# Optimization experiments

Hardware: AMD Instinct MI355X
Metric: run time of the kernel (lower is better)

## Reference

```python
import jax, jax.numpy as jnp
import numpy as np

# Model config (matches init_kwargs)
B, T, D = 2, 2048, 2048
H, KH, F = 16, 4, 8192
HD = D // H            # 128
G = H // KH            # q heads per kv head = 4
EPS = 1e-5


def _ln(x, g, b):
    m = jnp.mean(x, axis=-1, keepdims=True)
    v = jnp.mean((x - m) ** 2, axis=-1, keepdims=True)
    return (x - m) * jax.lax.rsqrt(v + EPS) * g + b


def setup_inputs() -> dict:
    key = jax.random.key(0)
    ks = jax.random.split(key, 8)

    def xav(k, shape):
        lim = (6.0 / (shape[0] + shape[1])) ** 0.5
        return jax.random.uniform(k, shape, jnp.float32, -lim, lim)

    x = jax.random.normal(ks[0], (B, T, D), jnp.float32)
    mask = jnp.tril(jnp.ones((1, 1, T, T), jnp.int32))  # causal
    # Linear weights stored as [in, out] (transpose of torch nn.Linear)
    return {
        "x": x,
        "mask": mask,
        "Wq": xav(ks[1], (D, H * HD)), "bq": jnp.zeros((H * HD,), jnp.float32),
        "Wk": xav(ks[2], (D, KH * HD)), "bk": jnp.zeros((KH * HD,), jnp.float32),
        "Wv": xav(ks[3], (D, KH * HD)), "bv": jnp.zeros((KH * HD,), jnp.float32),
        "Wo": xav(ks[4], (H * HD, D)), "bo": jnp.zeros((D,), jnp.float32),
        "ln1_g": jnp.ones((D,), jnp.float32), "ln1_b": jnp.zeros((D,), jnp.float32),
        "ln2_g": jnp.ones((D,), jnp.float32), "ln2_b": jnp.zeros((D,), jnp.float32),
        "fln_g": jnp.ones((D,), jnp.float32), "fln_b": jnp.zeros((D,), jnp.float32),
        "W1": xav(ks[5], (D, F)), "b1": jnp.zeros((F,), jnp.float32),
        "W2": xav(ks[6], (D, F)), "b2": jnp.zeros((F,), jnp.float32),
        "W3": xav(ks[7], (F, D)), "b3": jnp.zeros((D,), jnp.float32),
    }


def reference(x, mask, Wq, bq, Wk, bk, Wv, bv, Wo, bo,
              ln1_g, ln1_b, ln2_g, ln2_b, fln_g, fln_b,
              W1, b1, W2, b2, W3, b3):
    scale = 1.0 / np.sqrt(HD)
    # --- attention block (pre-LN + residual) ---
    h = _ln(x, ln1_g, ln1_b)
    q = (h @ Wq + bq).reshape(B, T, KH, G, HD)   # q head k*G+g uses kv head k
    k = (h @ Wk + bk).reshape(B, T, KH, HD)
    v = (h @ Wv + bv).reshape(B, T, KH, HD)
    # GQA scores without repeat_interleave: broadcast kv head across group g
    scores = jnp.einsum('btkgd,bskd->bkgts', q, k) * scale  # [B,KH,G,T,T]
    scores = jnp.clip(scores, -100.0, 100.0)
    scores = jnp.where(mask[:, :, None] == 0, -jnp.inf, scores)
    attn = jax.nn.softmax(scores, axis=-1)
    ctx = jnp.einsum('bkgts,bskd->btkgd', attn, v).reshape(B, T, H * HD)
    x = x + (ctx @ Wo + bo)  # dropout is identity in eval
    # --- ln2 then SwiGLU FFN (which has its own internal LN and residual
    # around the *post-ln2* activation, faithful to original) ---
    x = _ln(x, ln2_g, ln2_b)
    r = x
    h2 = _ln(x, fln_g, fln_b)
    g_pre = h2 @ W1 + b1
    gate = g_pre * jax.nn.sigmoid(jnp.clip(g_pre, -10.0, 10.0))
    hidden = h2 @ W2 + b2
    return r + ((gate * hidden) @ W3 + b3)
```

## Files before the change

kernel.cpp:

```cpp
#include <hip/hip_runtime.h>
#include <math.h>
#include <stdint.h>

typedef __bf16 bf16_t;
typedef __bf16 bf16x4 __attribute__((ext_vector_type(4)));
typedef __bf16 bf16x8 __attribute__((ext_vector_type(8)));
typedef float  f32x4  __attribute__((ext_vector_type(4)));

#define D_MODEL 2048
#define T_SEQ   2048
#define BATCH   2
#define NROWS   (BATCH*T_SEQ)
#define NHEAD   16
#define HDIM    128
#define KVH     4
#define KVD     (KVH*HDIM)
#define FDIM    8192
#define QKVN    3072

__device__ __forceinline__ bf16x8 mk8(bf16x4 lo, bf16x4 hi) {
  union { bf16x4 h[2]; bf16x8 v; } u;
  u.h[0] = lo; u.h[1] = hi; return u.v;
}

__device__ __forceinline__ void gl16(const bf16_t* g, bf16_t* l) {
  __builtin_amdgcn_global_load_lds(
      (const uint32_t __attribute__((address_space(1)))*)g,
      (uint32_t __attribute__((address_space(3)))*)l, 16, 0, 0);
}

__global__ __launch_bounds__(256)
void transpose_w(const float* __restrict__ in, bf16_t* __restrict__ outT, int K, int N)
{
  __shared__ __align__(16) bf16_t t[64][72];
  const int tid = threadIdx.x;
  const int k0 = blockIdx.y * 64, n0 = blockIdx.x * 64;
  const int tr = tid >> 4, tc = (tid & 15) * 4;
#pragma unroll
  for (int i = 0; i < 4; ++i) {
    f32x4 v = *(const f32x4*)(in + (size_t)(k0 + tr + 16 * i) * N + n0 + tc);
#pragma unroll
    for (int e = 0; e < 4; ++e) t[tr + 16 * i][tc + e] = (bf16_t)v[e];
  }
  __syncthreads();
#pragma unroll
  for (int s = 0; s < 2; ++s) {
    const int c = s * 256 + tid;
    const int n = c >> 3, c8 = (c & 7) * 8;
    bf16x8 o;
#pragma unroll
    for (int e = 0; e < 8; ++e) o[e] = t[c8 + e][n];
    *(bf16x8*)(outT + (size_t)(n0 + n) * K + k0 + c8) = o;
  }
}

__global__ __launch_bounds__(256)
void concat_bias(const float* __restrict__ a, const float* __restrict__ b,
                 const float* __restrict__ c, float* __restrict__ dst)
{
  const int i = blockIdx.x * 256 + threadIdx.x;
  if (i >= QKVN) return;
  dst[i] = (i < 2048) ? a[i] : (i < 2560) ? b[i - 2048] : c[i - 2560];
}

template<typename TI>
__global__ __launch_bounds__(256)
void ln_kernel(const TI* __restrict__ x, const float* __restrict__ g,
               const float* __restrict__ b, bf16_t* __restrict__ out)
{
  const int row = blockIdx.x;
  const int tid = threadIdx.x;
  const TI* xr = x + (size_t)row * D_MODEL;
  float vals[8];
  if constexpr (sizeof(TI) == 4) {
    f32x4 v0 = *(const f32x4*)(xr + tid * 8);
    f32x4 v1 = *(const f32x4*)(xr + tid * 8 + 4);
#pragma unroll
    for (int e = 0; e < 4; ++e) { vals[e] = v0[e]; vals[4 + e] = v1[e]; }
  } else {
    bf16x8 v = *(const bf16x8*)(xr + tid * 8);
#pragma unroll
    for (int e = 0; e < 8; ++e) vals[e] = (float)v[e];
  }
  float s = 0.f, s2 = 0.f;
#pragma unroll
  for (int e = 0; e < 8; ++e) { s += vals[e]; s2 += vals[e] * vals[e]; }
#pragma unroll
  for (int off = 1; off < 64; off <<= 1) { s += __shfl_xor(s, off); s2 += __shfl_xor(s2, off); }
  __shared__ float red[8];
  const int wid = tid >> 6, lane = tid & 63;
  if (lane == 0) { red[wid] = s; red[4 + wid] = s2; }
  __syncthreads();
  s  = red[0] + red[1] + red[2] + red[3];
  s2 = red[4] + red[5] + red[6] + red[7];
  const float mean = s * (1.f / D_MODEL);
  const float var  = s2 * (1.f / D_MODEL) - mean * mean;
  const float rstd = rsqrtf(var + 1e-5f);
  f32x4 g0 = *(const f32x4*)(g + tid * 8), g1 = *(const f32x4*)(g + tid * 8 + 4);
  f32x4 b0 = *(const f32x4*)(b + tid * 8), b1 = *(const f32x4*)(b + tid * 8 + 4);
  bf16x8 o;
#pragma unroll
  for (int e = 0; e < 4; ++e) {
    o[e]     = (bf16_t)((vals[e]     - mean) * rstd * g0[e] + b0[e]);
    o[4 + e] = (bf16_t)((vals[4 + e] - mean) * rstd * g1[e] + b1[e]);
  }
  *(bf16x8*)(out + (size_t)row * D_MODEL + tid * 8) = o;
}

__global__ __launch_bounds__(256)
void ln2_fused(const bf16_t* __restrict__ x, const float* __restrict__ g2,
               const float* __restrict__ b2, const float* __restrict__ gf,
               const float* __restrict__ bf_, bf16_t* __restrict__ rout,
               bf16_t* __restrict__ hout)
{
  const int row = blockIdx.x;
  const int tid = threadIdx.x;
  const int wid = tid >> 6, lane = tid & 63;
  __shared__ float red[8];
  const bf16_t* xr = x + (size_t)row * D_MODEL;
  bf16x8 v = *(const bf16x8*)(xr + tid * 8);
  float vals[8]; float s = 0.f, s2 = 0.f;
#pragma unroll
  for (int e = 0; e < 8; ++e) { vals[e] = (float)v[e]; s += vals[e]; s2 += vals[e] * vals[e]; }
#pragma unroll
  for (int off = 1; off < 64; off <<= 1) { s += __shfl_xor(s, off); s2 += __shfl_xor(s2, off); }
  if (lane == 0) { red[wid] = s; red[4 + wid] = s2; }
  __syncthreads();
  s  = red[0] + red[1] + red[2] + red[3];
  s2 = red[4] + red[5] + red[6] + red[7];
  float mean = s * (1.f / D_MODEL);
  float var  = s2 * (1.f / D_MODEL) - mean * mean;
  float rstd = rsqrtf(var + 1e-5f);
  f32x4 ga0 = *(const f32x4*)(g2 + tid * 8), ga1 = *(const f32x4*)(g2 + tid * 8 + 4);
  f32x4 ba0 = *(const f32x4*)(b2 + tid * 8), ba1 = *(const f32x4*)(b2 + tid * 8 + 4);
  float y[8];
#pragma unroll
  for (int e = 0; e < 4; ++e) {
    y[e]     = (vals[e]     - mean) * rstd * ga0[e] + ba0[e];
    y[4 + e] = (vals[4 + e] - mean) * rstd * ga1[e] + ba1[e];
  }
  bf16x8 o1;
#pragma unroll
  for (int e = 0; e < 8; ++e) o1[e] = (bf16_t)y[e];
  *(bf16x8*)(rout + (size_t)row * D_MODEL + tid * 8) = o1;
  s = 0.f; s2 = 0.f;
#pragma unroll
  for (int e = 0; e < 8; ++e) { s += y[e]; s2 += y[e] * y[e]; }
#pragma unroll
  for (int off = 1; off < 64; off <<= 1) { s += __shfl_xor(s, off); s2 += __shfl_xor(s2, off); }
  __syncthreads();
  if (lane == 0) { red[wid] = s; red[4 + wid] = s2; }
  __syncthreads();
  s  = red[0] + red[1] + red[2] + red[3];
  s2 = red[4] + red[5] + red[6] + red[7];
  mean = s * (1.f / D_MODEL);
  var  = s2 * (1.f / D_MODEL) - mean * mean;
  rstd = rsqrtf(var + 1e-5f);
  f32x4 gb0 = *(const f32x4*)(gf + tid * 8), gb1 = *(const f32x4*)(gf + tid * 8 + 4);
  f32x4 bb0 = *(const f32x4*)(bf_ + tid * 8), bb1 = *(const f32x4*)(bf_ + tid * 8 + 4);
  bf16x8 o2;
#pragma unroll
  for (int e = 0; e < 4; ++e) {
    o2[e]     = (bf16_t)((y[e]     - mean) * rstd * gb0[e] + bb0[e]);
    o2[4 + e] = (bf16_t)((y[4 + e] - mean) * rstd * gb1[e] + bb1[e]);
  }
  *(bf16x8*)(hout + (size_t)row * D_MODEL + tid * 8) = o2;
}

enum { EPI_NONE = 0, EPI_RES = 1, EPI_SILU = 2, EPI_MUL = 3 };

template<int EPI, int BM_T, typename TE, typename TO>
__global__ __launch_bounds__(512, 2)
void gemm8p(const bf16_t* __restrict__ A, const bf16_t* __restrict__ Bt,
            const float* __restrict__ bias, const TE* __restrict__ extra,
            TO* __restrict__ out, int M, int N, int K)
{
  constexpr int ALs = BM_T / 128;
  constexpr int RF  = BM_T / 32;
  __shared__ __align__(16) bf16_t As[2][2][BM_T * 32];
  __shared__ __align__(16) bf16_t Bs[2][2][256 * 32];
  const int tid = threadIdx.x, lane = tid & 63, wid = tid >> 6;
  const int wr = wid >> 2, wc = wid & 3;
  const int l16 = lane & 15, lq = lane >> 4;
  const int m0 = blockIdx.y * BM_T, n0 = blockIdx.x * 256;

  const bf16_t* aP[ALs]; int aL[ALs];
#pragma unroll
  for (int s = 0; s < ALs; ++s) {
    const int c = s * 512 + tid;
    const int row = c >> 2, pos = c & 3;
    aP[s] = A + (size_t)(m0 + row) * K + (pos ^ ((row >> 1) & 3)) * 8;
    aL[s] = (s * 512 + wid * 64) * 8;
  }
  const bf16_t* bP[2]; int bL[2];
#pragma unroll
  for (int s = 0; s < 2; ++s) {
    const int c = s * 512 + tid;
    const int row = c >> 2, pos = c & 3;
    bP[s] = Bt + (size_t)(n0 + row) * K + (pos ^ ((row >> 1) & 3)) * 8;
    bL[s] = (s * 512 + wid * 64) * 8;
  }

  int offA[RF];
#pragma unroll
  for (int i = 0; i < RF; ++i) {
    const int r = wr * (BM_T / 2) + i * 16 + l16;
    offA[i] = r * 32 + ((lq ^ ((r >> 1) & 3)) * 8);
  }
  int offB[4];
#pragma unroll
  for (int jj = 0; jj < 4; ++jj) {
    const int r = wc * 64 + jj * 16 + l16;
    offB[jj] = r * 32 + ((lq ^ ((r >> 1) & 3)) * 8);
  }

  f32x4 acc[RF][4];
#pragma unroll
  for (int i = 0; i < RF; ++i)
#pragma unroll
    for (int j = 0; j < 4; ++j) acc[i][j] = (f32x4){0.f, 0.f, 0.f, 0.f};

  auto SA = [&](int t, int bb, int kh) {
#pragma unroll
    for (int s = 0; s < ALs; ++s) gl16(aP[s] + t * 64 + kh * 32, &As[bb][kh][aL[s]]);
  };
  auto SB = [&](int t, int bb, int kh) {
#pragma unroll
    for (int s = 0; s < 2; ++s) gl16(bP[s] + t * 64 + kh * 32, &Bs[bb][kh][bL[s]]);
  };
#define BAR_()  __builtin_amdgcn_s_barrier()
#define LGKM_() do { asm volatile("s_waitcnt lgkmcnt(0)" ::: "memory"); \
                     __builtin_amdgcn_sched_barrier(0); } while (0)

  const int nt = K >> 6;
  SA(0, 0, 0); SB(0, 0, 0); SA(0, 0, 1); SB(0, 0, 1);
  if (nt > 1) { SA(1, 1, 0); SB(1, 1, 0); SA(1, 1, 1); }
  if (nt > 2) {
    if constexpr (ALs == 2) asm volatile("s_waitcnt vmcnt(6)" ::: "memory");
    else                    asm volatile("s_waitcnt vmcnt(4)" ::: "memory");
  } else {
    asm volatile("s_waitcnt vmcnt(0)" ::: "memory");
  }
  BAR_();

  for (int t = 0; t < nt; ++t) {
    const int b = t & 1, ob = b ^ 1;
    const bool s1 = (t + 1 < nt), s2 = (t + 2 < nt);
    bf16x8 af[RF], bf0, bf1;
#pragma unroll
    for (int i = 0; i < RF; ++i) af[i] = *(const bf16x8*)(&As[b][0][offA[i]]);
    bf0 = *(const bf16x8*)(&Bs[b][0][offB[0]]);
    bf1 = *(const bf16x8*)(&Bs[b][0][offB[1]]);
    if (s1) SB(t + 1, ob, 1);
    BAR_(); LGKM_();
    __builtin_amdgcn_s_setprio(1);
#pragma unroll
    for (int i = 0; i < RF; ++i) {
      acc[i][0] = __builtin_amdgcn_mfma_f32_16x16x32_bf16(af[i], bf0, acc[i][0], 0, 0, 0);
      acc[i][1] = __builtin_amdgcn_mfma_f32_16x16x32_bf16(af[i], bf1, acc[i][1], 0, 0, 0);
    }
    __builtin_amdgcn_s_setprio(0);
    BAR_();
    bf0 = *(const bf16x8*)(&Bs[b][0][offB[2]]);
    bf1 = *(const bf16x8*)(&Bs[b][0][offB[3]]);
    if (s2) SA(t + 2, b, 0);
    BAR_(); LGKM_();
    __builtin_amdgcn_s_setprio(1);
#pragma unroll
    for (int i = 0; i < RF; ++i) {
      acc[i][2] = __builtin_amdgcn_mfma_f32_16x16x32_bf16(af[i], bf0, acc[i][2], 0, 0, 0);
      acc[i][3] = __builtin_amdgcn_mfma_f32_16x16x32_bf16(af[i], bf1, acc[i][3], 0, 0, 0);
    }
    __builtin_amdgcn_s_setprio(0);
    BAR_();
#pragma unroll
    for (int i = 0; i < RF; ++i) af[i] = *(const bf16x8*)(&As[b][1][offA[i]]);
    bf0 = *(const bf16x8*)(&Bs[b][1][offB[0]]);
    bf1 = *(const bf16x8*)(&Bs[b][1][offB[1]]);
    if (s2) SB(t + 2, b, 0);
    BAR_(); LGKM_();
    __builtin_amdgcn_s_setprio(1);
#pragma unroll
    for (int i = 0; i < RF; ++i) {
      acc[i][0] = __builtin_amdgcn_mfma_f32_16x16x32_bf16(af[i], bf0, acc[i][0], 0, 0, 0);
      acc[i][1] = __builtin_amdgcn_mfma_f32_16x16x32_bf16(af[i], bf1, acc[i][1], 0, 0, 0);
    }
    __builtin_amdgcn_s_setprio(0);
    BAR_();
    bf0 = *(const bf16x8*)(&Bs[b][1][offB[2]]);
    bf1 = *(const bf16x8*)(&Bs[b][1][offB[3]]);
    if (s2) SA(t + 2, b, 1);
    BAR_(); LGKM_();
    __builtin_amdgcn_s_setprio(1);
#pragma unroll
    for (int i = 0; i < RF; ++i) {
      acc[i][2] = __builtin_amdgcn_mfma_f32_16x16x32_bf16(af[i], bf0, acc[i][2], 0, 0, 0);
      acc[i][3] = __builtin_amdgcn_mfma_f32_16x16x32_bf16(af[i], bf1, acc[i][3], 0, 0, 0);
    }
    __builtin_amdgcn_s_setprio(0);
    if (t < nt - 2) {
      if constexpr (ALs == 2) asm volatile("s_waitcnt vmcnt(6)" ::: "memory");
      else                    asm volatile("s_waitcnt vmcnt(4)" ::: "memory");
    } else {
      asm volatile("s_waitcnt vmcnt(0)" ::: "memory");
    }
    BAR_();
  }
#undef BAR_
#undef LGKM_

#pragma unroll
  for (int j = 0; j < 4; ++j) {
    const int col = n0 + wc * 64 + j * 16 + l16;
    const float bb = bias[col];
#pragma unroll
    for (int i = 0; i < RF; ++i) {
      const int row0 = m0 + wr * (BM_T / 2) + i * 16 + lq * 4;
#pragma unroll
      for (int e = 0; e < 4; ++e) {
        const size_t idx = (size_t)(row0 + e) * N + col;
        float vv = acc[i][j][e] + bb;
        if (EPI == EPI_RES)       vv += (float)extra[idx];
        else if (EPI == EPI_SILU) { float c2 = fminf(fmaxf(vv, -10.f), 10.f); vv = vv / (1.f + __expf(-c2)); }
        else if (EPI == EPI_MUL)  vv *= (float)extra[idx];
        out[idx] = (TO)vv;
      }
    }
  }
}

template<int EPI, typename TE, typename TO>
__global__ __launch_bounds__(256)
void gemm_kernel(const bf16_t* __restrict__ A, const float* __restrict__ W,
                 const float* __restrict__ bias, const TE* __restrict__ extra,
                 TO* __restrict__ out, int M, int N, int K)
{
  __shared__ bf16_t As[128][40];
  __shared__ bf16_t Bs[128][40];
  const int tid  = threadIdx.x;
  const int lane = tid & 63, wid = tid >> 6;
  const int wr = wid >> 1, wc = wid & 1;
  const int l16 = lane & 15, lq = lane >> 4;
  const int m0 = blockIdx.y * 128, n0 = blockIdx.x * 128;

  f32x4 acc[4][4];
#pragma unroll
  for (int i = 0; i < 4; ++i)
#pragma unroll
    for (int j = 0; j < 4; ++j) acc[i][j] = (f32x4){0.f, 0.f, 0.f, 0.f};

  const int ar = tid >> 1, ah = tid & 1;
  const int kk = tid & 31, cc = tid >> 5;

  for (int k0 = 0; k0 < K; k0 += 32) {
    const bf16_t* asrc = A + (size_t)(m0 + ar) * K + k0 + ah * 16;
    *(bf16x8*)(&As[ar][ah * 16])     = *(const bf16x8*)(asrc);
    *(bf16x8*)(&As[ar][ah * 16 + 8]) = *(const bf16x8*)(asrc + 8);
    const float* wsrc = W + (size_t)(k0 + kk) * N + n0;
#pragma unroll
    for (int it = 0; it < 2; ++it) {
      const int c = cc * 8 + it * 64;
      f32x4 wa = *(const f32x4*)(wsrc + c);
      f32x4 wb = *(const f32x4*)(wsrc + c + 4);
#pragma unroll
      for (int e = 0; e < 4; ++e) {
        Bs[c + e][kk]     = (bf16_t)wa[e];
        Bs[c + 4 + e][kk] = (bf16_t)wb[e];
      }
    }
    __syncthreads();
    bf16x8 af[4], bfr[4];
#pragma unroll
    for (int i = 0; i < 4; ++i) {
      const bf16_t* p = &As[wr * 64 + i * 16 + l16][lq * 4];
      af[i] = mk8(*(const bf16x4*)p, *(const bf16x4*)(p + 16));
    }
#pragma unroll
    for (int j = 0; j < 4; ++j) {
      const bf16_t* p = &Bs[wc * 64 + j * 16 + l16][lq * 4];
      bfr[j] = mk8(*(const bf16x4*)p, *(const bf16x4*)(p + 16));
    }
#pragma unroll
    for (int i = 0; i < 4; ++i)
#pragma unroll
      for (int j = 0; j < 4; ++j)
        acc[i][j] = __builtin_amdgcn_mfma_f32_16x16x32_bf16(af[i], bfr[j], acc[i][j], 0, 0, 0);
    __syncthreads();
  }

#pragma unroll
  for (int j = 0; j < 4; ++j) {
    const int col = n0 + wc * 64 + j * 16 + l16;
    const float bb = bias[col];
#pragma unroll
    for (int i = 0; i < 4; ++i) {
      const int row0 = m0 + wr * 64 + i * 16 + lq * 4;
#pragma unroll
      for (int e = 0; e < 4; ++e) {
        const size_t idx = (size_t)(row0 + e) * N + col;
        float vv = acc[i][j][e] + bb;
        if (EPI == EPI_RES)       vv += (float)extra[idx];
        else if (EPI == EPI_SILU) { float c2 = fminf(fmaxf(vv, -10.f), 10.f); vv = vv / (1.f + __expf(-c2)); }
        else if (EPI == EPI_MUL)  vv *= (float)extra[idx];
        out[idx] = (TO)vv;
      }
    }
  }
}

__global__ __launch_bounds__(256)
void attn_kernel(const bf16_t* __restrict__ q, const bf16_t* __restrict__ k,
                 const bf16_t* __restrict__ v, bf16_t* __restrict__ ctx,
                 int q_ld, int kv_ld)
{
  __shared__ __align__(16) bf16_t Ks[64 * 128];
  __shared__ __align__(16) bf16_t Vt[128][72];

  const int tid = threadIdx.x, lane = tid & 63, wid = tid >> 6;
  const int l16 = lane & 15, lq = lane >> 4;
  const int bh = blockIdx.y;
  const int b = bh >> 4, h = bh & 15;
  const int kh = h >> 2;
  const float scale = 0.08838834764831845f;

  for (int pass = 0; pass < 2; ++pass) {
    const int qt = pass ? blockIdx.x : (31 - blockIdx.x);
    const int qbase = qt * 64;
    const int qrow = qbase + wid * 16 + l16;

    const bf16_t* qp = q + (size_t)(b * T_SEQ + qrow) * q_ld + h * HDIM;
    bf16x8 bq[4];
#pragma unroll
    for (int s = 0; s < 4; ++s) bq[s] = *(const bf16x8*)(qp + s * 32 + lq * 8);

    float m_r = -1e30f, l_r = 0.f;
    f32x4 acc_o[8];
#pragma unroll
    for (int jh = 0; jh < 8; ++jh) acc_o[jh] = (f32x4){0.f, 0.f, 0.f, 0.f};

    const int ntiles = qt + 1;
    for (int t = 0; t < ntiles; ++t) {
      const int kb = t * 64;
      __syncthreads();
#pragma unroll
      for (int it = 0; it < 4; ++it) {
        const int c = it * 256 + tid;
        const int kvr = c >> 4, pos = c & 15;
        const int src = pos ^ (kvr & 7);
        gl16(k + (size_t)(b * T_SEQ + kb + kvr) * kv_ld + kh * HDIM + src * 8,
             Ks + (size_t)(it * 256 + wid * 64) * 8);
      }
#pragma unroll
      for (int it = 0; it < 4; ++it) {
        const int c = tid + it * 256;
        const int r = c & 63, voff = (c >> 6) * 8;
        bf16x8 vv = *(const bf16x8*)(v + (size_t)(b * T_SEQ + kb + r) * kv_ld + kh * HDIM + voff);
#pragma unroll
        for (int e = 0; e < 8; ++e) Vt[voff + e][r] = vv[e];
      }
      __syncthreads();

      f32x4 sf[4];
#pragma unroll
      for (int j = 0; j < 4; ++j) {
        sf[j] = (f32x4){0.f, 0.f, 0.f, 0.f};
        const int kvr = j * 16 + l16;
#pragma unroll
        for (int s = 0; s < 4; ++s) {
          bf16x8 ak = *(const bf16x8*)(Ks + kvr * 128 + (((s * 4 + lq) ^ (kvr & 7)) * 8));
          sf[j] = __builtin_amdgcn_mfma_f32_16x16x32_bf16(ak, bq[s], sf[j], 0, 0, 0);
        }
      }

      float p[4][4];
      float tmax = -1e30f;
#pragma unroll
      for (int j = 0; j < 4; ++j)
#pragma unroll
        for (int e = 0; e < 4; ++e) {
          const int kvc = kb + j * 16 + lq * 4 + e;
          float sv = sf[j][e] * scale;
          sv = fminf(fmaxf(sv, -100.f), 100.f);
          if (kvc > qrow) sv = -1e30f;
          p[j][e] = sv;
          tmax = fmaxf(tmax, sv);
        }
      tmax = fmaxf(tmax, __shfl_xor(tmax, 16));
      tmax = fmaxf(tmax, __shfl_xor(tmax, 32));
      const float mnew = fmaxf(m_r, tmax);
      const float resc = __expf(m_r - mnew);
      m_r = mnew;
      float rsum = 0.f;
#pragma unroll
      for (int j = 0; j < 4; ++j)
#pragma unroll
        for (int e = 0; e < 4; ++e) {
          p[j][e] = __expf(p[j][e] - m_r);
          rsum += p[j][e];
        }
      rsum += __shfl_xor(rsum, 16);
      rsum += __shfl_xor(rsum, 32);
      l_r = l_r * resc + rsum;

      float resc4[4];
#pragma unroll
      for (int e = 0; e < 4; ++e) resc4[e] = __shfl(resc, lq * 4 + e);
#pragma unroll
      for (int jh = 0; jh < 8; ++jh)
#pragma unroll
        for (int e = 0; e < 4; ++e) acc_o[jh][e] *= resc4[e];

      bf16x8 pa[2];
#pragma unroll
      for (int sk = 0; sk < 2; ++sk) {
        bf16x4 lo, hi;
#pragma unroll
        for (int e = 0; e < 4; ++e) { lo[e] = (bf16_t)p[2 * sk][e]; hi[e] = (bf16_t)p[2 * sk + 1][e]; }
        pa[sk] = mk8(lo, hi);
      }
#pragma unroll
      for (int jh = 0; jh < 8; ++jh) {
#pragma unroll
        for (int sk = 0; sk < 2; ++sk) {
          const bf16_t* pV = &Vt[jh * 16 + l16][sk * 32 + lq * 4];
          bf16x8 bv2 = mk8(*(const bf16x4*)pV, *(const bf16x4*)(pV + 16));
          acc_o[jh] = __builtin_amdgcn_mfma_f32_16x16x32_bf16(pa[sk], bv2, acc_o[jh], 0, 0, 0);
        }
      }
    }

    float l4[4];
#pragma unroll
    for (int e = 0; e < 4; ++e) l4[e] = __shfl(l_r, lq * 4 + e);
    bf16_t* op = ctx + (size_t)(b * T_SEQ + qbase + wid * 16) * D_MODEL + h * HDIM;
#pragma unroll
    for (int jh = 0; jh < 8; ++jh)
#pragma unroll
      for (int e = 0; e < 4; ++e)
        op[(size_t)(lq * 4 + e) * D_MODEL + jh * 16 + l16] = (bf16_t)(acc_o[jh][e] / l4[e]);
  }
}

extern "C" void kernel_launch(void* const* d_in, const int* in_sizes, int n_in,
                              void* d_out, int out_size, void* d_ws, size_t ws_size,
                              hipStream_t stream)
{
  const float* x   = (const float*)d_in[0];
  const float* Wq  = (const float*)d_in[2];
  const float* bq  = (const float*)d_in[3];
  const float* Wk  = (const float*)d_in[4];
  const float* bk  = (const float*)d_in[5];
  const float* Wv  = (const float*)d_in[6];
  const float* bv  = (const float*)d_in[7];
  const float* Wo  = (const float*)d_in[8];
  const float* bo  = (const float*)d_in[9];
  const float* g1  = (const float*)d_in[10];
  const float* b1n = (const float*)d_in[11];
  const float* g2  = (const float*)d_in[12];
  const float* b2n = (const float*)d_in[13];
  const float* gf  = (const float*)d_in[14];
  const float* bfn = (const float*)d_in[15];
  const float* W1  = (const float*)d_in[16];
  const float* bb1 = (const float*)d_in[17];
  const float* W2  = (const float*)d_in[18];
  const float* bb2 = (const float*)d_in[19];
  const float* W3  = (const float*)d_in[20];
  const float* bb3 = (const float*)d_in[21];
  float* out = (float*)d_out;

  char* ws = (char*)d_ws;
  size_t off = 0;
  auto alloc = [&](size_t bytes) -> void* {
    void* p = ws + off; off += (bytes + 255) & ~(size_t)255; return p;
  };
  const dim3 blk(256);

  bf16_t* Wt_qkv = (bf16_t*)alloc((size_t)QKVN * D_MODEL * 2);
  bf16_t* Wt_o   = (bf16_t*)alloc((size_t)D_MODEL * D_MODEL * 2);
  bf16_t* Wt1    = (bf16_t*)alloc((size_t)FDIM * D_MODEL * 2);
  bf16_t* Wt2    = (bf16_t*)alloc((size_t)FDIM * D_MODEL * 2);
  bf16_t* Wt3    = (bf16_t*)alloc((size_t)D_MODEL * FDIM * 2);
  float*  bqkv   = (float*)alloc((size_t)QKVN * 4);
  bf16_t* hbuf   = (bf16_t*)alloc((size_t)NROWS * D_MODEL * 2);
  bf16_t* qkvbuf = (bf16_t*)alloc((size_t)NROWS * QKVN * 2);
  bf16_t* rbuf   = (bf16_t*)alloc((size_t)NROWS * D_MODEL * 2);
  bf16_t* h2buf  = (bf16_t*)alloc((size_t)NROWS * D_MODEL * 2);
  const size_t core = off;

  if (core <= ws_size) {
    size_t avail = ws_size - core;
    int chunk = (int)((avail / ((size_t)FDIM * 2)) & ~(size_t)255);
    bf16_t* gbuf;
    if (chunk >= 256) { gbuf = (bf16_t*)(ws + core); if (chunk > NROWS) chunk = NROWS; }
    else              { gbuf = qkvbuf; chunk = 1536; }
    bf16_t* x1buf = qkvbuf;

    transpose_w<<<dim3(32, 32),  blk, 0, stream>>>(Wq, Wt_qkv, D_MODEL, 2048);
    transpose_w<<<dim3(8, 32),   blk, 0, stream>>>(Wk, Wt_qkv + (size_t)2048 * D_MODEL, D_MODEL, 512);
    transpose_w<<<dim3(8, 32),   blk, 0, stream>>>(Wv, Wt_qkv + (size_t)2560 * D_MODEL, D_MODEL, 512);
    transpose_w<<<dim3(32, 32),  blk, 0, stream>>>(Wo, Wt_o, D_MODEL, D_MODEL);
    transpose_w<<<dim3(128, 32), blk, 0, stream>>>(W1, Wt1, D_MODEL, FDIM);
    transpose_w<<<dim3(128, 32), blk, 0, stream>>>(W2, Wt2, D_MODEL, FDIM);
    transpose_w<<<dim3(32, 128), blk, 0, stream>>>(W3, Wt3, FDIM, D_MODEL);
    concat_bias<<<12, blk, 0, stream>>>(bq, bk, bv, bqkv);

    ln_kernel<float><<<NROWS, blk, 0, stream>>>(x, g1, b1n, hbuf);
    gemm8p<EPI_NONE, 256, bf16_t, bf16_t><<<dim3(QKVN / 256, NROWS / 256), 512, 0, stream>>>(
        hbuf, Wt_qkv, bqkv, nullptr, qkvbuf, NROWS, QKVN, D_MODEL);
    attn_kernel<<<dim3(16, 32), blk, 0, stream>>>(
        qkvbuf, qkvbuf + 2048, qkvbuf + 2560, hbuf, QKVN, QKVN);
    gemm8p<EPI_RES, 128, float, bf16_t><<<dim3(D_MODEL / 256, NROWS / 128), 512, 0, stream>>>(
        hbuf, Wt_o, bo, x, x1buf, NROWS, D_MODEL, D_MODEL);
    ln2_fused<<<NROWS, blk, 0, stream>>>(x1buf, g2, b2n, gf, bfn, rbuf, h2buf);

    for (int r0 = 0; r0 < NROWS; r0 += chunk) {
      const int rows = (NROWS - r0 < chunk) ? (NROWS - r0) : chunk;
      gemm8p<EPI_SILU, 256, bf16_t, bf16_t><<<dim3(FDIM / 256, rows / 256), 512, 0, stream>>>(
          h2buf + (size_t)r0 * D_MODEL, Wt1, bb1, nullptr, gbuf, rows, FDIM, D_MODEL);
      gemm8p<EPI_MUL, 256, bf16_t, bf16_t><<<dim3(FDIM / 256, rows / 256), 512, 0, stream>>>(
          h2buf + (size_t)r0 * D_MODEL, Wt2, bb2, gbuf, gbuf, rows, FDIM, D_MODEL);
      gemm8p<EPI_RES, 128, bf16_t, float><<<dim3(D_MODEL / 256, rows / 128), 512, 0, stream>>>(
          gbuf, Wt3, bb3, rbuf + (size_t)r0 * D_MODEL, out + (size_t)r0 * D_MODEL, rows, D_MODEL, FDIM);
    }
    return;
  }

  off = 0;
  const size_t DBYTES = (size_t)NROWS * D_MODEL * 2;
  bf16_t* fhbuf  = (bf16_t*)alloc(DBYTES);
  bf16_t* fqbuf  = (bf16_t*)alloc(DBYTES);
  bf16_t* fkbuf  = (bf16_t*)alloc((size_t)NROWS * KVD * 2);
  bf16_t* fvbuf  = (bf16_t*)alloc((size_t)NROWS * KVD * 2);
  bf16_t* frbuf  = (bf16_t*)alloc(DBYTES);
  bf16_t* fh2buf = (bf16_t*)alloc(DBYTES);
  const size_t base = off;
  size_t avail = (ws_size > base) ? (ws_size - base) : 0;
  int chunk = (int)((avail / ((size_t)FDIM * 2)) & ~(size_t)127);
  bf16_t* gbuf;
  if (chunk >= 128) { gbuf = (bf16_t*)(ws + base); if (chunk > NROWS) chunk = NROWS; }
  else              { gbuf = fqbuf; chunk = 1024; }

  ln_kernel<float><<<NROWS, blk, 0, stream>>>(x, g1, b1n, fhbuf);
  gemm_kernel<EPI_NONE, bf16_t, bf16_t><<<dim3(16, 32), blk, 0, stream>>>(fhbuf, Wq, bq, nullptr, fqbuf, NROWS, 2048, 2048);
  gemm_kernel<EPI_NONE, bf16_t, bf16_t><<<dim3(4, 32),  blk, 0, stream>>>(fhbuf, Wk, bk, nullptr, fkbuf, NROWS, 512, 2048);
  gemm_kernel<EPI_NONE, bf16_t, bf16_t><<<dim3(4, 32),  blk, 0, stream>>>(fhbuf, Wv, bv, nullptr, fvbuf, NROWS, 512, 2048);
  attn_kernel<<<dim3(16, 32), blk, 0, stream>>>(fqbuf, fkbuf, fvbuf, fhbuf, 2048, 512);
  gemm_kernel<EPI_RES, float, bf16_t><<<dim3(16, 32), blk, 0, stream>>>(fhbuf, Wo, bo, x, fqbuf, NROWS, 2048, 2048);
  ln_kernel<bf16_t><<<NROWS, blk, 0, stream>>>(fqbuf, g2, b2n, frbuf);
  ln_kernel<bf16_t><<<NROWS, blk, 0, stream>>>(frbuf, gf, bfn, fh2buf);
  for (int r0 = 0; r0 < NROWS; r0 += chunk) {
    const int rows = (NROWS - r0 < chunk) ? (NROWS - r0) : chunk;
    gemm_kernel<EPI_SILU, bf16_t, bf16_t><<<dim3(64, rows / 128), blk, 0, stream>>>(
        fh2buf + (size_t)r0 * D_MODEL, W1, bb1, nullptr, gbuf, rows, FDIM, 2048);
    gemm_kernel<EPI_MUL, bf16_t, bf16_t><<<dim3(64, rows / 128), blk, 0, stream>>>(
        fh2buf + (size_t)r0 * D_MODEL, W2, bb2, gbuf, gbuf, rows, FDIM, 2048);
    gemm_kernel<EPI_RES, bf16_t, float><<<dim3(16, rows / 128), blk, 0, stream>>>(
        gbuf, W3, bb3, frbuf + (size_t)r0 * D_MODEL, out + (size_t)r0 * D_MODEL, rows, 2048, FDIM);
  }
}
```

Before: 896.7 us.

## Add XCD-aware block swizzle and dedicated 128x256 GEMM kernel for N=2048 projections

Adds a block-index remap that spreads consecutive workgroups across the eight XCDs so neighbouring tiles share L2, applied to every gemm8p launch. Adds a new gemm2p kernel for 128-row tiles with a simpler two-half-K pipeline, explicit barriers and lgkm waits, and uses it for the output projection and the W3 down projection. The aim is better L2 reuse and a tighter load/MFMA schedule for the N=2048 GEMMs. The swizzle assumes the grid block count divides evenly by 8.

```diff
diff --git a/kernel.cpp b/kernel.cpp
--- a/kernel.cpp
+++ b/kernel.cpp
@@ -169,6 +169,13 @@
 
 enum { EPI_NONE = 0, EPI_RES = 1, EPI_SILU = 2, EPI_MUL = 3 };
 
+__device__ __forceinline__ void xcd_swz(int BMv, int BNv, int& m0, int& n0) {
+  const int nbx = gridDim.x, nwg = nbx * gridDim.y;
+  int flat = blockIdx.y * nbx + blockIdx.x;
+  flat = (flat & 7) * (nwg >> 3) + (flat >> 3);
+  m0 = (flat / nbx) * BMv; n0 = (flat % nbx) * BNv;
+}
+
 template<int EPI, int BM_T, typename TE, typename TO>
 __global__ __launch_bounds__(512, 2)
 void gemm8p(const bf16_t* __restrict__ A, const bf16_t* __restrict__ Bt,
@@ -182,7 +189,7 @@
   const int tid = threadIdx.x, lane = tid & 63, wid = tid >> 6;
   const int wr = wid >> 2, wc = wid & 3;
   const int l16 = lane & 15, lq = lane >> 4;
-  const int m0 = blockIdx.y * BM_T, n0 = blockIdx.x * 256;
+  int m0, n0; xcd_swz(BM_T, 256, m0, n0);
 
   const bf16_t* aP[ALs]; int aL[ALs];
 #pragma unroll
@@ -306,8 +313,6 @@
     }
     BAR_();
   }
-#undef BAR_
-#undef LGKM_
 
 #pragma unroll
   for (int j = 0; j < 4; ++j) {
@@ -316,6 +321,130 @@
 #pragma unroll
     for (int i = 0; i < RF; ++i) {
       const int row0 = m0 + wr * (BM_T / 2) + i * 16 + lq * 4;
+#pragma unroll
+      for (int e = 0; e < 4; ++e) {
+        const size_t idx = (size_t)(row0 + e) * N + col;
+        float vv = acc[i][j][e] + bb;
+        if (EPI == EPI_RES)       vv += (float)extra[idx];
+        else if (EPI == EPI_SILU) { float c2 = fminf(fmaxf(vv, -10.f), 10.f); vv = vv / (1.f + __expf(-c2)); }
+        else if (EPI == EPI_MUL)  vv *= (float)extra[idx];
+        out[idx] = (TO)vv;
+      }
+    }
+  }
+}
+
+template<int EPI, typename TE, typename TO>
+__global__ __launch_bounds__(512, 2)
+void gemm2p(const bf16_t* __restrict__ A, const bf16_t* __restrict__ Bt,
+            const float* __restrict__ bias, const TE* __restrict__ extra,
+            TO* __restrict__ out, int M, int N, int K)
+{
+  __shared__ __align__(16) bf16_t As[2][2][128 * 32];
+  __shared__ __align__(16) bf16_t Bs[2][2][256 * 32];
+  const int tid = threadIdx.x, lane = tid & 63, wid = tid >> 6;
+  const int wr = wid >> 2, wc = wid & 3;
+  const int l16 = lane & 15, lq = lane >> 4;
+  int m0, n0; xcd_swz(128, 256, m0, n0);
+
+  const bf16_t* aP; int aL;
+  {
+    const int row = tid >> 2, pos = tid & 3;
+    aP = A + (size_t)(m0 + row) * K + (pos ^ ((row >> 1) & 3)) * 8;
+    aL = (wid * 64) * 8;
+  }
+  const bf16_t* bP[2]; int bL[2];
+#pragma unroll
+  for (int s = 0; s < 2; ++s) {
+    const int c = s * 512 + tid;
+    const int row = c >> 2, pos = c & 3;
+    bP[s] = Bt + (size_t)(n0 + row) * K + (pos ^ ((row >> 1) & 3)) * 8;
+    bL[s] = (s * 512 + wid * 64) * 8;
+  }
+
+  int offA[4], offB[4];
+#pragma unroll
+  for (int i = 0; i < 4; ++i) {
+    const int r = wr * 64 + i * 16 + l16;
+    offA[i] = r * 32 + ((lq ^ ((r >> 1) & 3)) * 8);
+  }
+#pragma unroll
+  for (int j = 0; j < 4; ++j) {
+    const int r = wc * 64 + j * 16 + l16;
+    offB[j] = r * 32 + ((lq ^ ((r >> 1) & 3)) * 8);
+  }
+
+  f32x4 acc[4][4];
+#pragma unroll
+  for (int i = 0; i < 4; ++i)
+#pragma unroll
+    for (int j = 0; j < 4; ++j) acc[i][j] = (f32x4){0.f, 0.f, 0.f, 0.f};
+
+  auto SA = [&](int t, int bb, int kh) { gl16(aP + t * 64 + kh * 32, &As[bb][kh][aL]); };
+  auto SB = [&](int t, int bb, int kh) {
+#pragma unroll
+    for (int s = 0; s < 2; ++s) gl16(bP[s] + t * 64 + kh * 32, &Bs[bb][kh][bL[s]]);
+  };
+
+  const int nt = K >> 6;
+  SA(0, 0, 0); SB(0, 0, 0); SA(0, 0, 1); SB(0, 0, 1);
+  if (nt > 1) {
+    SA(1, 1, 0); SB(1, 1, 0);
+    asm volatile("s_waitcnt vmcnt(3)" ::: "memory");
+  } else {
+    asm volatile("s_waitcnt vmcnt(0)" ::: "memory");
+  }
+  __builtin_amdgcn_s_barrier();
+
+  for (int t = 0; t < nt; ++t) {
+    const int b = t & 1, ob = b ^ 1;
+    bf16x8 af[4], bfr[4];
+#pragma unroll
+    for (int i = 0; i < 4; ++i) af[i]  = *(const bf16x8*)(&As[b][0][offA[i]]);
+#pragma unroll
+    for (int j = 0; j < 4; ++j) bfr[j] = *(const bf16x8*)(&Bs[b][0][offB[j]]);
+    if (t + 1 < nt) { SA(t + 1, ob, 1); SB(t + 1, ob, 1); }
+    __builtin_amdgcn_s_barrier();
+    asm volatile("s_waitcnt lgkmcnt(0)" ::: "memory");
+    __builtin_amdgcn_sched_barrier(0);
+    __builtin_amdgcn_s_setprio(1);
+#pragma unroll
+    for (int i = 0; i < 4; ++i)
+#pragma unroll
+      for (int j = 0; j < 4; ++j)
+        acc[i][j] = __builtin_amdgcn_mfma_f32_16x16x32_bf16(af[i], bfr[j], acc[i][j], 0, 0, 0);
+    __builtin_amdgcn_s_setprio(0);
+    __builtin_amdgcn_s_barrier();
+#pragma unroll
+    for (int i = 0; i < 4; ++i) af[i]  = *(const bf16x8*)(&As[b][1][offA[i]]);
+#pragma unroll
+    for (int j = 0; j < 4; ++j) bfr[j] = *(const bf16x8*)(&Bs[b][1][offB[j]]);
+    if (t + 2 < nt) {
+      SA(t + 2, b, 0); SB(t + 2, b, 0);
+      asm volatile("s_waitcnt vmcnt(3)" ::: "memory");
+    } else {
+      asm volatile("s_waitcnt vmcnt(0)" ::: "memory");
+    }
+    __builtin_amdgcn_s_barrier();
+    asm volatile("s_waitcnt lgkmcnt(0)" ::: "memory");
+    __builtin_amdgcn_sched_barrier(0);
+    __builtin_amdgcn_s_setprio(1);
+#pragma unroll
+    for (int i = 0; i < 4; ++i)
+#pragma unroll
+      for (int j = 0; j < 4; ++j)
+        acc[i][j] = __builtin_amdgcn_mfma_f32_16x16x32_bf16(af[i], bfr[j], acc[i][j], 0, 0, 0);
+    __builtin_amdgcn_s_setprio(0);
+    __builtin_amdgcn_s_barrier();
+  }
+
+#pragma unroll
+  for (int j = 0; j < 4; ++j) {
+    const int col = n0 + wc * 64 + j * 16 + l16;
+    const float bb = bias[col];
+#pragma unroll
+    for (int i = 0; i < 4; ++i) {
+      const int row0 = m0 + wr * 64 + i * 16 + lq * 4;
 #pragma unroll
       for (int e = 0; e < 4; ++e) {
         const size_t idx = (size_t)(row0 + e) * N + col;
@@ -609,7 +738,7 @@
         hbuf, Wt_qkv, bqkv, nullptr, qkvbuf, NROWS, QKVN, D_MODEL);
     attn_kernel<<<dim3(16, 32), blk, 0, stream>>>(
         qkvbuf, qkvbuf + 2048, qkvbuf + 2560, hbuf, QKVN, QKVN);
-    gemm8p<EPI_RES, 128, float, bf16_t><<<dim3(D_MODEL / 256, NROWS / 128), 512, 0, stream>>>(
+    gemm2p<EPI_RES, float, bf16_t><<<dim3(D_MODEL / 256, NROWS / 128), 512, 0, stream>>>(
         hbuf, Wt_o, bo, x, x1buf, NROWS, D_MODEL, D_MODEL);
     ln2_fused<<<NROWS, blk, 0, stream>>>(x1buf, g2, b2n, gf, bfn, rbuf, h2buf);
 
@@ -619,7 +748,7 @@
           h2buf + (size_t)r0 * D_MODEL, Wt1, bb1, nullptr, gbuf, rows, FDIM, D_MODEL);
       gemm8p<EPI_MUL, 256, bf16_t, bf16_t><<<dim3(FDIM / 256, rows / 256), 512, 0, stream>>>(
           h2buf + (size_t)r0 * D_MODEL, Wt2, bb2, gbuf, gbuf, rows, FDIM, D_MODEL);
-      gemm8p<EPI_RES, 128, bf16_t, float><<<dim3(D_MODEL / 256, rows / 128), 512, 0, stream>>>(
+      gemm2p<EPI_RES, bf16_t, float><<<dim3(D_MODEL / 256, rows / 128), 512, 0, stream>>>(
           gbuf, Wt3, bb3, rbuf + (size_t)r0 * D_MODEL, out + (size_t)r0 * D_MODEL, rows, D_MODEL, FDIM);
     }
     return;
```

Measured after the change: 900.6 us. Within noise of the previous version (+0.4%).
